# Kernel optimization log

Measured on AMD Instinct MI355X. Metric: run time of the kernel, lower is better.

Reference implementation:

```python
import jax, jax.numpy as jnp
import numpy as np

B, N, H = 2, 8192, 128
EPS = 1e-06


def setup_inputs() -> dict:
    key = jax.random.key(0)
    k1, k2, k3, k4 = jax.random.split(key, 4)
    x = jax.random.normal(k1, (B, N, H), dtype=jnp.float32)
    # adjacency is sparse in the original (tf.sparse); represented dense here
    # for the reference math (same result as sparse_dense_matmul).
    adj = jax.random.normal(k2, (B, N, N), dtype=jnp.float32)
    W = jax.random.normal(k3, (H, H), dtype=jnp.float32)
    b = jax.random.normal(k4, (H,), dtype=jnp.float32)
    return {"x": x, "adj": adj, "W": W, "b": b}


def reference(x, adj, W, b):
    # in-degree over |adj|, per batch, per node: [B, N]
    in_degrees = jnp.sum(jnp.abs(adj), axis=-1)
    # symmetric-ish degree normalization: [B, N, 1]
    norm = jnp.power(in_degrees + EPS, -0.5)[..., None]
    # dense projection: [B, N, H]
    support = jnp.matmul(x, W)
    # batched SpMM (dense equivalent) with pre/post degree norm
    out = jnp.einsum("bmn,bnh->bmh", adj, support * norm) * norm
    return jax.nn.elu(out + b)
```

## Files before the change

### kernel.cpp

```cpp
#include <hip/hip_runtime.h>
#include <hip/hip_bf16.h>
#include <math.h>

#define NN 8192
#define HD 128
#define NB 2
#define EPSF 1e-6f
#define BM 32
#define BK 128
#define NSTEP (NN / BK)

typedef __attribute__((ext_vector_type(8))) __bf16 bf16x8;
typedef __attribute__((ext_vector_type(4))) float f32x4;

__global__ __launch_bounds__(256) void k_degree(const float* __restrict__ adj,
                                                float* __restrict__ norm) {
    const int row  = blockIdx.x * 4 + (threadIdx.x >> 6);
    const int lane = threadIdx.x & 63;
    const float4* p = (const float4*)(adj + (size_t)row * NN);
    float s = 0.f;
#pragma unroll
    for (int i = 0; i < 32; ++i) {
        float4 v = p[(size_t)i * 64 + lane];
        s += fabsf(v.x) + fabsf(v.y) + fabsf(v.z) + fabsf(v.w);
    }
#pragma unroll
    for (int off = 32; off > 0; off >>= 1) s += __shfl_down(s, off);
    if (lane == 0) norm[row] = rsqrtf(s + EPSF);
}

__global__ __launch_bounds__(256) void k_support(const float* __restrict__ x,
                                                 const float* __restrict__ W,
                                                 const float* __restrict__ norm,
                                                 __hip_bfloat16* __restrict__ snT) {
    const int b  = blockIdx.x >> 9;
    const int n0 = (blockIdx.x & 511) * 16;
    __shared__ float xs[16][132];
    const int t = threadIdx.x;
    {
        const int r = t >> 4, c0 = (t & 15) * 8;
        const float* src = x + ((size_t)(b * NN + n0 + r)) * HD + c0;
        *(float4*)&xs[r][c0]     = *(const float4*)src;
        *(float4*)&xs[r][c0 + 4] = *(const float4*)(src + 4);
    }
    __syncthreads();
    const int nl = t & 15;
    const int h0 = (t >> 4) * 8;
    float s[8] = {0.f,0.f,0.f,0.f,0.f,0.f,0.f,0.f};
#pragma unroll 4
    for (int k = 0; k < HD; ++k) {
        const float xv = xs[nl][k];
        const float* wr = W + k * HD + h0;
        float4 wa = *(const float4*)wr;
        float4 wb = *(const float4*)(wr + 4);
        s[0] += xv * wa.x; s[1] += xv * wa.y; s[2] += xv * wa.z; s[3] += xv * wa.w;
        s[4] += xv * wb.x; s[5] += xv * wb.y; s[6] += xv * wb.z; s[7] += xv * wb.w;
    }
    const float nv = norm[b * NN + n0 + nl];
#pragma unroll
    for (int hb = 0; hb < 8; ++hb)
        snT[((size_t)b * HD + h0 + hb) * NN + n0 + nl] = __float2bfloat16(s[hb] * nv);
}

__device__ __forceinline__ bf16x8 cvt8(float4 a, float4 b) {
    bf16x8 r;
    r[0] = (__bf16)a.x; r[1] = (__bf16)a.y; r[2] = (__bf16)a.z; r[3] = (__bf16)a.w;
    r[4] = (__bf16)b.x; r[5] = (__bf16)b.y; r[6] = (__bf16)b.z; r[7] = (__bf16)b.w;
    return r;
}

__device__ __forceinline__ void gload_lds16(const float* g, void* l) {
    __builtin_amdgcn_global_load_lds(
        (const __attribute__((address_space(1))) void*)g,
        (__attribute__((address_space(3))) void*)l, 16, 0, 0);
}

__global__ __launch_bounds__(256, 2) void k_gemm9(const float* __restrict__ adj,
                                                  const __hip_bfloat16* __restrict__ snT,
                                                  const float* __restrict__ norm,
                                                  const float* __restrict__ bias,
                                                  float* __restrict__ out) {
    const int b    = blockIdx.y;
    const int swz  = (blockIdx.x & 7) * 32 + (blockIdx.x >> 3);
    const int m0   = swz * BM;
    const int w    = threadIdx.x >> 6;
    const int lane = threadIdx.x & 63;
    const int fr   = lane & 15;
    const int g    = lane >> 4;

    const float* adjB = adj + (size_t)b * NN * NN;
    const __hip_bfloat16* snB = snT + (size_t)b * HD * NN;

    __shared__ __align__(16) char Abuf[4][BM * BK * 4];

    const float* sptr[4];
#pragma unroll
    for (int c = 0; c < 4; ++c) {
        const int fg   = (w * 4 + c) * 64 + lane;
        const int row  = fg >> 5;
        const int gsrc = (fg & 31) ^ (row & 7);
        sptr[c] = adjB + (size_t)(m0 + row) * NN + gsrc * 4;
    }

    const __hip_bfloat16* bp0 = snB + (size_t)(w * 32 + fr) * NN + g * 8;
    const __hip_bfloat16* bp1 = bp0 + (size_t)16 * NN;

    f32x4 acc[2][2] = {};
    const int xr = fr & 7;
    bf16x8 BfA[2][4], BfB[2][4];

#define STAGE(idx) do {                                                       \
        char* nb_ = Abuf[(idx) & 3];                                          \
        _Pragma("unroll")                                                     \
        for (int c = 0; c < 4; ++c)                                           \
            gload_lds16(sptr[c] + (idx) * BK, &nb_[(w * 4 + c) * 1024]);      \
    } while (0)
#define LOADB(BX, idx) do {                                                   \
        _Pragma("unroll")                                                     \
        for (int ks = 0; ks < 4; ++ks) {                                      \
            BX[0][ks] = *(const bf16x8*)(bp0 + (idx) * BK + ks * 32);         \
            BX[1][ks] = *(const bf16x8*)(bp1 + (idx) * BK + ks * 32);         \
        }                                                                     \
    } while (0)
#define WAITN(n) asm volatile("s_waitcnt vmcnt(" #n ")" ::: "memory")
#define BAR() do { __builtin_amdgcn_s_barrier();                              \
                   __builtin_amdgcn_sched_barrier(0); } while (0)
#define COMPUTE(kidx, BX) do {                                                \
        const char* lb_ = Abuf[(kidx) & 3];                                   \
        _Pragma("unroll")                                                     \
        for (int mt = 0; mt < 2; ++mt) {                                      \
            const char* rbase_ = lb_ + (mt * 16 + fr) * 512;                  \
            _Pragma("unroll")                                                 \
            for (int ks = 0; ks < 4; ++ks) {                                  \
                float4 fa_ = *(const float4*)(rbase_ + ((ks * 8 + ((g * 2 + 0) ^ xr)) << 4)); \
                float4 fb_ = *(const float4*)(rbase_ + ((ks * 8 + ((g * 2 + 1) ^ xr)) << 4)); \
                bf16x8 af_ = cvt8(fa_, fb_);                                  \
                acc[mt][0] = __builtin_amdgcn_mfma_f32_16x16x32_bf16(af_, BX[0][ks], acc[mt][0], 0, 0, 0); \
                acc[mt][1] = __builtin_amdgcn_mfma_f32_16x16x32_bf16(af_, BX[1][ks], acc[mt][1], 0, 0, 0); \
            }                                                                 \
        }                                                                     \
    } while (0)

    STAGE(0);
    STAGE(1);
    LOADB(BfA, 0);

#pragma unroll 1
    for (int k = 0; k < NSTEP - 3; k += 2) {
        LOADB(BfB, k + 1);
        STAGE(k + 2);
        WAITN(16); BAR();
        COMPUTE(k, BfA);

        LOADB(BfA, k + 2);
        STAGE(k + 3);
        WAITN(16); BAR();
        COMPUTE(k + 1, BfB);
    }

    LOADB(BfB, NSTEP - 1);
    WAITN(0); BAR();
    COMPUTE(NSTEP - 2, BfA);

    WAITN(0); BAR();
    COMPUTE(NSTEP - 1, BfB);

#undef STAGE
#undef LOADB
#undef WAITN
#undef BAR
#undef COMPUTE

    const float* normB = norm + b * NN + m0;
    float* outB = out + ((size_t)b * NN + m0) * HD;
#pragma unroll
    for (int mt = 0; mt < 2; ++mt)
#pragma unroll
        for (int ht = 0; ht < 2; ++ht) {
            const int h  = w * 32 + ht * 16 + fr;
            const float bv = bias[h];
#pragma unroll
            for (int j = 0; j < 4; ++j) {
                const int r = mt * 16 + g * 4 + j;
                float v = acc[mt][ht][j] * normB[r] + bv;
                v = v > 0.f ? v : expm1f(v);
                outB[(size_t)r * HD + h] = v;
            }
        }
}

extern "C" void kernel_launch(void* const* d_in, const int* in_sizes, int n_in,
                              void* d_out, int out_size, void* d_ws, size_t ws_size,
                              hipStream_t stream) {
    (void)in_sizes; (void)n_in; (void)out_size; (void)ws_size;
    const float* x    = (const float*)d_in[0];
    const float* adj  = (const float*)d_in[1];
    const float* W    = (const float*)d_in[2];
    const float* bias = (const float*)d_in[3];
    float* out = (float*)d_out;

    float* norm = (float*)d_ws;
    __hip_bfloat16* snT = (__hip_bfloat16*)((char*)d_ws + 65536);

    k_degree <<<dim3(NB * NN / 4),  dim3(256), 0, stream>>>(adj, norm);
    k_support<<<dim3(NB * NN / 16), dim3(256), 0, stream>>>(x, W, norm, snT);
    k_gemm9  <<<dim3(NN / BM, NB),  dim3(256), 0, stream>>>(adj, snT, norm, bias, out);
}
```

Before: 274.6 us.

## Cast adjacency to bf16 in the degree pass and stream bf16 into GEMM

The degree kernel now also writes a bf16 copy of the adjacency matrix. The GEMM then loads that half-width copy straight into LDS, with no fp32-to-bf16 conversion in its inner loop. The GEMM is also restructured to 512 threads, a K-tile of 256 and a single-buffered B fragment, with each wave covering 16 output columns. Total memory traffic stays about the same, since the extra 256 MB bf16 write replaces half of the second fp32 read, and the change needs a large workspace.

```diff
diff --git a/kernel.cpp b/kernel.cpp
--- a/kernel.cpp
+++ b/kernel.cpp
@@ -7,22 +7,32 @@
 #define NB 2
 #define EPSF 1e-6f
 #define BM 32
-#define BK 128
-#define NSTEP (NN / BK)
+#define BKE 256
+#define NSTEP (NN / BKE)
 
 typedef __attribute__((ext_vector_type(8))) __bf16 bf16x8;
+typedef __attribute__((ext_vector_type(4))) __bf16 bf16x4;
 typedef __attribute__((ext_vector_type(4))) float f32x4;
 
-__global__ __launch_bounds__(256) void k_degree(const float* __restrict__ adj,
-                                                float* __restrict__ norm) {
+__global__ __launch_bounds__(256) void k_degcast(const float* __restrict__ adj,
+                                                 float* __restrict__ norm,
+                                                 __hip_bfloat16* __restrict__ adjh) {
     const int row  = blockIdx.x * 4 + (threadIdx.x >> 6);
     const int lane = threadIdx.x & 63;
     const float4* p = (const float4*)(adj + (size_t)row * NN);
+    bf16x4* q = (bf16x4*)(adjh + (size_t)row * NN);
     float s = 0.f;
 #pragma unroll
-    for (int i = 0; i < 32; ++i) {
-        float4 v = p[(size_t)i * 64 + lane];
-        s += fabsf(v.x) + fabsf(v.y) + fabsf(v.z) + fabsf(v.w);
+    for (int i = 0; i < 16; ++i) {
+        float4 a = p[i * 128 + lane];
+        float4 b = p[i * 128 + 64 + lane];
+        s += fabsf(a.x) + fabsf(a.y) + fabsf(a.z) + fabsf(a.w)
+           + fabsf(b.x) + fabsf(b.y) + fabsf(b.z) + fabsf(b.w);
+        bf16x4 ha, hb;
+        ha[0] = (__bf16)a.x; ha[1] = (__bf16)a.y; ha[2] = (__bf16)a.z; ha[3] = (__bf16)a.w;
+        hb[0] = (__bf16)b.x; hb[1] = (__bf16)b.y; hb[2] = (__bf16)b.z; hb[3] = (__bf16)b.w;
+        q[i * 128 + lane]      = ha;
+        q[i * 128 + 64 + lane] = hb;
     }
 #pragma unroll
     for (int off = 32; off > 0; off >>= 1) s += __shfl_down(s, off);
@@ -62,24 +72,17 @@
         snT[((size_t)b * HD + h0 + hb) * NN + n0 + nl] = __float2bfloat16(s[hb] * nv);
 }
 
-__device__ __forceinline__ bf16x8 cvt8(float4 a, float4 b) {
-    bf16x8 r;
-    r[0] = (__bf16)a.x; r[1] = (__bf16)a.y; r[2] = (__bf16)a.z; r[3] = (__bf16)a.w;
-    r[4] = (__bf16)b.x; r[5] = (__bf16)b.y; r[6] = (__bf16)b.z; r[7] = (__bf16)b.w;
-    return r;
-}
-
-__device__ __forceinline__ void gload_lds16(const float* g, void* l) {
+__device__ __forceinline__ void gload_lds16(const void* g, void* l) {
     __builtin_amdgcn_global_load_lds(
         (const __attribute__((address_space(1))) void*)g,
         (__attribute__((address_space(3))) void*)l, 16, 0, 0);
 }
 
-__global__ __launch_bounds__(256, 2) void k_gemm9(const float* __restrict__ adj,
-                                                  const __hip_bfloat16* __restrict__ snT,
-                                                  const float* __restrict__ norm,
-                                                  const float* __restrict__ bias,
-                                                  float* __restrict__ out) {
+__global__ __launch_bounds__(512, 4) void k_gemm10(const __hip_bfloat16* __restrict__ adjh,
+                                                   const __hip_bfloat16* __restrict__ snT,
+                                                   const float* __restrict__ norm,
+                                                   const float* __restrict__ bias,
+                                                   float* __restrict__ out) {
     const int b    = blockIdx.y;
     const int swz  = (blockIdx.x & 7) * 32 + (blockIdx.x >> 3);
     const int m0   = swz * BM;
@@ -87,83 +90,74 @@
     const int lane = threadIdx.x & 63;
     const int fr   = lane & 15;
     const int g    = lane >> 4;
-
-    const float* adjB = adj + (size_t)b * NN * NN;
-    const __hip_bfloat16* snB = snT + (size_t)b * HD * NN;
-
-    __shared__ __align__(16) char Abuf[4][BM * BK * 4];
-
-    const float* sptr[4];
-#pragma unroll
-    for (int c = 0; c < 4; ++c) {
-        const int fg   = (w * 4 + c) * 64 + lane;
+    const int xr   = fr & 7;
+
+    const __hip_bfloat16* adjB = adjh + (size_t)b * NN * NN;
+    const __hip_bfloat16* snB  = snT  + (size_t)b * HD * NN;
+
+    __shared__ __align__(16) char Abuf[4][BM * BKE * 2];
+
+    const __hip_bfloat16* sp[2];
+#pragma unroll
+    for (int c = 0; c < 2; ++c) {
+        const int fg   = (w * 2 + c) * 64 + lane;
         const int row  = fg >> 5;
-        const int gsrc = (fg & 31) ^ (row & 7);
-        sptr[c] = adjB + (size_t)(m0 + row) * NN + gsrc * 4;
-    }
-
-    const __hip_bfloat16* bp0 = snB + (size_t)(w * 32 + fr) * NN + g * 8;
-    const __hip_bfloat16* bp1 = bp0 + (size_t)16 * NN;
-
-    f32x4 acc[2][2] = {};
-    const int xr = fr & 7;
-    bf16x8 BfA[2][4], BfB[2][4];
+        const int slot = (fg & 31) ^ (row & 7);
+        sp[c] = adjB + (size_t)(m0 + row) * NN + slot * 8;
+    }
+
+    const __hip_bfloat16* bp = snB + (size_t)(w * 16 + fr) * NN + g * 8;
+
+    f32x4 acc[2] = {};
+    bf16x8 Bf[8];
 
 #define STAGE(idx) do {                                                       \
         char* nb_ = Abuf[(idx) & 3];                                          \
         _Pragma("unroll")                                                     \
-        for (int c = 0; c < 4; ++c)                                           \
-            gload_lds16(sptr[c] + (idx) * BK, &nb_[(w * 4 + c) * 1024]);      \
+        for (int c = 0; c < 2; ++c)                                           \
+            gload_lds16(sp[c] + (size_t)(idx) * BKE, &nb_[(w * 2 + c) * 1024]); \
     } while (0)
-#define LOADB(BX, idx) do {                                                   \
+#define LOADB(idx) do {                                                       \
         _Pragma("unroll")                                                     \
-        for (int ks = 0; ks < 4; ++ks) {                                      \
-            BX[0][ks] = *(const bf16x8*)(bp0 + (idx) * BK + ks * 32);         \
-            BX[1][ks] = *(const bf16x8*)(bp1 + (idx) * BK + ks * 32);         \
-        }                                                                     \
+        for (int ks = 0; ks < 8; ++ks)                                        \
+            Bf[ks] = *(const bf16x8*)(bp + (size_t)(idx) * BKE + ks * 32);    \
     } while (0)
 #define WAITN(n) asm volatile("s_waitcnt vmcnt(" #n ")" ::: "memory")
 #define BAR() do { __builtin_amdgcn_s_barrier();                              \
                    __builtin_amdgcn_sched_barrier(0); } while (0)
-#define COMPUTE(kidx, BX) do {                                                \
+#define COMPUTE(kidx) do {                                                    \
         const char* lb_ = Abuf[(kidx) & 3];                                   \
         _Pragma("unroll")                                                     \
         for (int mt = 0; mt < 2; ++mt) {                                      \
             const char* rbase_ = lb_ + (mt * 16 + fr) * 512;                  \
             _Pragma("unroll")                                                 \
-            for (int ks = 0; ks < 4; ++ks) {                                  \
-                float4 fa_ = *(const float4*)(rbase_ + ((ks * 8 + ((g * 2 + 0) ^ xr)) << 4)); \
-                float4 fb_ = *(const float4*)(rbase_ + ((ks * 8 + ((g * 2 + 1) ^ xr)) << 4)); \
-                bf16x8 af_ = cvt8(fa_, fb_);                                  \
-                acc[mt][0] = __builtin_amdgcn_mfma_f32_16x16x32_bf16(af_, BX[0][ks], acc[mt][0], 0, 0, 0); \
-                acc[mt][1] = __builtin_amdgcn_mfma_f32_16x16x32_bf16(af_, BX[1][ks], acc[mt][1], 0, 0, 0); \
+            for (int ks = 0; ks < 8; ++ks) {                                  \
+                bf16x8 af_ = *(const bf16x8*)(rbase_ + (((ks * 4 + g) ^ xr) << 4)); \
+                acc[mt] = __builtin_amdgcn_mfma_f32_16x16x32_bf16(af_, Bf[ks], acc[mt], 0, 0, 0); \
             }                                                                 \
         }                                                                     \
     } while (0)
 
     STAGE(0);
     STAGE(1);
-    LOADB(BfA, 0);
 
 #pragma unroll 1
-    for (int k = 0; k < NSTEP - 3; k += 2) {
-        LOADB(BfB, k + 1);
+    for (int k = 0; k < NSTEP - 2; ++k) {
+        LOADB(k);
+        WAITN(10);
+        BAR();
         STAGE(k + 2);
-        WAITN(16); BAR();
-        COMPUTE(k, BfA);
-
-        LOADB(BfA, k + 2);
-        STAGE(k + 3);
-        WAITN(16); BAR();
-        COMPUTE(k + 1, BfB);
-    }
-
-    LOADB(BfB, NSTEP - 1);
-    WAITN(0); BAR();
-    COMPUTE(NSTEP - 2, BfA);
-
-    WAITN(0); BAR();
-    COMPUTE(NSTEP - 1, BfB);
+        __builtin_amdgcn_sched_barrier(0);
+        COMPUTE(k);
+    }
+
+    LOADB(NSTEP - 2);
+    WAITN(10); BAR();
+    COMPUTE(NSTEP - 2);
+
+    LOADB(NSTEP - 1);
+    WAITN(8);  BAR();
+    COMPUTE(NSTEP - 1);
 
 #undef STAGE
 #undef LOADB
@@ -173,19 +167,16 @@
 
     const float* normB = norm + b * NN + m0;
     float* outB = out + ((size_t)b * NN + m0) * HD;
+    const int h  = w * 16 + fr;
+    const float bv = bias[h];
 #pragma unroll
     for (int mt = 0; mt < 2; ++mt)
 #pragma unroll
-        for (int ht = 0; ht < 2; ++ht) {
-            const int h  = w * 32 + ht * 16 + fr;
-            const float bv = bias[h];
-#pragma unroll
-            for (int j = 0; j < 4; ++j) {
-                const int r = mt * 16 + g * 4 + j;
-                float v = acc[mt][ht][j] * normB[r] + bv;
-                v = v > 0.f ? v : expm1f(v);
-                outB[(size_t)r * HD + h] = v;
-            }
+        for (int j = 0; j < 4; ++j) {
+            const int r = mt * 16 + g * 4 + j;
+            float v = acc[mt][j] * normB[r] + bv;
+            v = v > 0.f ? v : expm1f(v);
+            outB[(size_t)r * HD + h] = v;
         }
 }
 
@@ -200,9 +191,10 @@
     float* out = (float*)d_out;
 
     float* norm = (float*)d_ws;
-    __hip_bfloat16* snT = (__hip_bfloat16*)((char*)d_ws + 65536);
-
-    k_degree <<<dim3(NB * NN / 4),  dim3(256), 0, stream>>>(adj, norm);
+    __hip_bfloat16* snT  = (__hip_bfloat16*)((char*)d_ws + 65536);
+    __hip_bfloat16* adjh = (__hip_bfloat16*)((char*)d_ws + 65536 + (4 << 20));
+
+    k_degcast<<<dim3(NB * NN / 4),  dim3(256), 0, stream>>>(adj, norm, adjh);
     k_support<<<dim3(NB * NN / 16), dim3(256), 0, stream>>>(x, W, norm, snT);
-    k_gemm9  <<<dim3(NN / BM, NB),  dim3(256), 0, stream>>>(adj, snT, norm, bias, out);
-}
+    k_gemm10 <<<dim3(NN / BM, NB),  dim3(512), 0, stream>>>(adjh, snT, norm, bias, out);
+}
```

Measured after the change: 315.1 us. 1.15x slower.
